# Performance work log

Measured on AMD Instinct MI355X. Metric: run time of the kernel, lower is better.

## Reference

```python
import jax, jax.numpy as jnp
import numpy as np

N_NODES = 100000
N_EDGES = 1600000
IN_F = 128
HID = 16
NEG_SLOPE = 0.2


def setup_inputs() -> dict:
    key = jax.random.key(0)
    ks = jax.random.split(key, 12)
    x = jax.random.normal(ks[0], (N_NODES, IN_F), dtype=jnp.float32)
    edge_index = jax.random.randint(ks[1], (2, N_EDGES), 0, N_NODES, dtype=jnp.int32)
    s1 = 1.0 / np.sqrt(IN_F)
    s2 = 1.0 / np.sqrt(2 * HID)
    # layer 1: heads=2, out=16, concat -> 32
    W1 = jax.random.normal(ks[2], (IN_F, 2 * HID), dtype=jnp.float32) * s1
    a_src1 = jax.random.normal(ks[3], (2, HID), dtype=jnp.float32) * s2
    a_dst1 = jax.random.normal(ks[4], (2, HID), dtype=jnp.float32) * s2
    b1 = jnp.zeros((2 * HID,), dtype=jnp.float32)
    # layer 2: heads=1, out=1
    W2 = jax.random.normal(ks[5], (2 * HID, 1), dtype=jnp.float32) * s2
    a_src2 = jax.random.normal(ks[6], (1, 1), dtype=jnp.float32)
    a_dst2 = jax.random.normal(ks[7], (1, 1), dtype=jnp.float32)
    b2 = jnp.zeros((1,), dtype=jnp.float32)
    return {"x": x, "edge_index": edge_index, "W1": W1, "a_src1": a_src1,
            "a_dst1": a_dst1, "b1": b1, "W2": W2, "a_src2": a_src2,
            "a_dst2": a_dst2, "b2": b2}


def gat_conv(x, src, dst, W, a_src, a_dst, bias, heads, out_ch, concat):
    # PyG GATConv: linear proj, per-edge leaky-relu score, segment softmax over
    # incoming edges (dst), scatter-add aggregation. Self loops already in src/dst.
    n = x.shape[0]
    h = (x @ W).reshape(n, heads, out_ch)                      # [N,H,C]
    alpha_s = (h * a_src[None]).sum(-1)                        # [N,H]
    alpha_d = (h * a_dst[None]).sum(-1)                        # [N,H]
    e = jax.nn.leaky_relu(alpha_s[src] + alpha_d[dst], NEG_SLOPE)  # [E,H]
    m = jax.lax.stop_gradient(jax.ops.segment_max(e, dst, num_segments=n))
    ex = jnp.exp(e - m[dst])
    denom = jax.ops.segment_sum(ex, dst, num_segments=n)       # [N,H]
    alpha = ex / (denom[dst] + 1e-16)                          # [E,H]
    out = jax.ops.segment_sum(alpha[..., None] * h[src], dst, num_segments=n)  # [N,H,C]
    out = out.reshape(n, heads * out_ch) if concat else out.mean(axis=1)
    return out + bias


def reference(x, edge_index, W1, a_src1, a_dst1, b1, W2, a_src2, a_dst2, b2):
    n = x.shape[0]
    loop = jnp.arange(n, dtype=edge_index.dtype)
    src = jnp.concatenate([edge_index[0], loop])
    dst = jnp.concatenate([edge_index[1], loop])
    h = jax.nn.elu(gat_conv(x, src, dst, W1, a_src1, a_dst1, b1, 2, HID, True))
    out = gat_conv(h, src, dst, W2, a_src2, a_dst2, b2, 1, 1, False)
    return out
```

## Files before the change

### kernel.cpp

```cpp
#include <hip/hip_runtime.h>
#include <math.h>

#define IN_F 128
#define C1 32
#define NEG 0.2f
#define BSZ 128
#define CAP 2560
#define EPB 2048
#define TPW 2

typedef _Float16 h16;
typedef _Float16 h16x2 __attribute__((ext_vector_type(2)));
typedef _Float16 h16x4 __attribute__((ext_vector_type(4)));
typedef _Float16 h16x8 __attribute__((ext_vector_type(8)));
typedef float f32x4 __attribute__((ext_vector_type(4)));

__device__ __forceinline__ float leaky(float x) { return x >= 0.f ? x : NEG * x; }

__global__ __launch_bounds__(256)
void k_fat(const float* __restrict__ x, const float* __restrict__ W1,
           const float* __restrict__ a_s, const float* __restrict__ a_d,
           h16* __restrict__ h1h, float* __restrict__ as1,
           float* __restrict__ ad1, int N,
           const int* __restrict__ ei, int E, int ET, int nbk,
           int* __restrict__ bcnt, int* __restrict__ ebuf, int nproj) {
    __shared__ int smem[6144];
    int t = threadIdx.x;
    if ((int)blockIdx.x < nproj) {
        int wid = t >> 6, lane = t & 63;
        int q = lane >> 4, r = lane & 15;
        h16x8 Bf[2][4];
        #pragma unroll
        for (int ct = 0; ct < 2; ++ct)
            #pragma unroll
            for (int kc = 0; kc < 4; ++kc)
                #pragma unroll
                for (int j = 0; j < 8; ++j)
                    Bf[ct][kc][j] = (h16)W1[(kc * 32 + q * 8 + j) * C1 + ct * 16 + r];
        float a_s0 = a_s[r], a_s1v = a_s[16 + r];
        float a_d0 = a_d[r], a_d1v = a_d[16 + r];
        #pragma unroll
        for (int tt = 0; tt < TPW; ++tt) {
            int tile = (blockIdx.x * 4 + wid) * TPW + tt;
            int m0 = tile << 4;
            if (m0 >= N) break;
            int row = m0 + r; if (row >= N) row = N - 1;
            const float* xr = x + (size_t)row * IN_F + q * 8;
            f32x4 acc0 = {0.f, 0.f, 0.f, 0.f};
            f32x4 acc1 = {0.f, 0.f, 0.f, 0.f};
            #pragma unroll
            for (int kc = 0; kc < 4; ++kc) {
                float4 xa = *(const float4*)(xr + kc * 32);
                float4 xb = *(const float4*)(xr + kc * 32 + 4);
                h16x8 A;
                A[0] = (h16)xa.x; A[1] = (h16)xa.y; A[2] = (h16)xa.z; A[3] = (h16)xa.w;
                A[4] = (h16)xb.x; A[5] = (h16)xb.y; A[6] = (h16)xb.z; A[7] = (h16)xb.w;
                acc0 = __builtin_amdgcn_mfma_f32_16x16x32_f16(A, Bf[0][kc], acc0, 0, 0, 0);
                acc1 = __builtin_amdgcn_mfma_f32_16x16x32_f16(A, Bf[1][kc], acc1, 0, 0, 0);
            }
            #pragma unroll
            for (int reg = 0; reg < 4; ++reg) {
                int node = m0 + q * 4 + reg;
                bool vld = node < N;
                float h0 = acc0[reg], h1 = acc1[reg];
                if (vld) {
                    h1h[(size_t)node * C1 + r]      = (h16)h0;
                    h1h[(size_t)node * C1 + 16 + r] = (h16)h1;
                }
                float s0 = h0 * a_s0, s1 = h1 * a_s1v;
                float d0 = h0 * a_d0, d1 = h1 * a_d1v;
                s0 += __shfl_xor(s0, 1); s0 += __shfl_xor(s0, 2); s0 += __shfl_xor(s0, 4); s0 += __shfl_xor(s0, 8);
                s1 += __shfl_xor(s1, 1); s1 += __shfl_xor(s1, 2); s1 += __shfl_xor(s1, 4); s1 += __shfl_xor(s1, 8);
                d0 += __shfl_xor(d0, 1); d0 += __shfl_xor(d0, 2); d0 += __shfl_xor(d0, 4); d0 += __shfl_xor(d0, 8);
                d1 += __shfl_xor(d1, 1); d1 += __shfl_xor(d1, 2); d1 += __shfl_xor(d1, 4); d1 += __shfl_xor(d1, 8);
                if (vld && r == 0) {
                    *(float2*)&as1[node * 2] = make_float2(s0, s1);
                    *(float2*)&ad1[node * 2] = make_float2(d0, d1);
                }
            }
        }
    } else {
        int* hist = smem;
        int* lcur = hist + 1024;
        int2* ecache = (int2*)(lcur + 1024);
        int bid = blockIdx.x - nproj;
        hist[t] = 0; hist[t + 256] = 0; hist[t + 512] = 0; hist[t + 768] = 0;
        __syncthreads();
        int i0 = bid * EPB, i1 = min(ET, i0 + EPB);
        for (int i = i0 + t; i < i1; i += 256) {
            int s, d;
            if (i < E) { s = ei[i]; d = ei[E + i]; } else { s = d = i - E; }
            ecache[i - i0] = make_int2(s, d);
            atomicAdd(&hist[d >> 7], 1);
        }
        __syncthreads();
        for (int b = t; b < nbk; b += 256) {
            int h = hist[b];
            int base = h ? atomicAdd(&bcnt[b], h) : 0;
            lcur[b] = b * CAP + base;
        }
        __syncthreads();
        for (int i = i0 + t; i < i1; i += 256) {
            int2 e = ecache[i - i0];
            int bkt = e.y >> 7;
            int pos = atomicAdd(&lcur[bkt], 1);
            if (pos < (bkt + 1) * CAP)
                ebuf[pos] = (e.x << 7) | (e.y & 127);
        }
    }
}

__global__ __launch_bounds__(512)
void k_bagg(const int* __restrict__ bcnt, const int* __restrict__ ebuf,
            int N, int nbk, int ET,
            const float* __restrict__ as1, const float* __restrict__ ad1,
            const float* __restrict__ b1, const float* __restrict__ W2,
            const h16* __restrict__ h1h, int* __restrict__ off,
            int* __restrict__ csr1, float* __restrict__ p2) {
    __shared__ int2 elist[CAP];
    __shared__ int deg[BSZ], sst[BSZ], cur[BSZ];
    __shared__ float adl[BSZ * 2];
    __shared__ int red[8];
    int b = blockIdx.x, t = threadIdx.x;
    int cnt = min(bcnt[b], CAP);
    int ebase = b * CAP;
    int n0 = b * BSZ;
    int part = 0;
    for (int k = t; k < b; k += 512) part += min(bcnt[k], CAP);
    part += __shfl_xor(part, 1);  part += __shfl_xor(part, 2);
    part += __shfl_xor(part, 4);  part += __shfl_xor(part, 8);
    part += __shfl_xor(part, 16); part += __shfl_xor(part, 32);
    if ((t & 63) == 0) red[t >> 6] = part;
    if (t < BSZ) {
        deg[t] = 0;
        int n = n0 + t;
        float2 v = (n < N) ? ((const float2*)ad1)[n] : make_float2(0.f, 0.f);
        adl[t * 2] = v.x; adl[t * 2 + 1] = v.y;
    }
    __syncthreads();
    int fbase = red[0] + red[1] + red[2] + red[3] + red[4] + red[5] + red[6] + red[7];
    if (b == nbk - 1 && t == 0) off[N] = ET;
    for (int i = t; i < cnt; i += 512)
        atomicAdd(&deg[ebuf[ebase + i] & 127], 1);
    __syncthreads();
    int v = (t < BSZ) ? deg[t] : 0;
    __syncthreads();
    for (int o = 1; o < BSZ; o <<= 1) {
        int xv = (t >= o && t < BSZ) ? deg[t - o] : 0;
        __syncthreads();
        if (t < BSZ) deg[t] += xv;
        __syncthreads();
    }
    if (t < BSZ) {
        int excl = deg[t] - v;
        sst[t] = excl; cur[t] = excl;
        if (n0 + t < N) off[n0 + t] = fbase + excl;
    }
    __syncthreads();
    for (int i = t; i < cnt; i += 512) {
        int e = ebuf[ebase + i];
        int dl = e & 127, s = e >> 7;
        float2 asv = ((const float2*)as1)[s];
        float w0 = __expf(leaky(asv.x + adl[dl * 2 + 0]));
        float w1 = __expf(leaky(asv.y + adl[dl * 2 + 1]));
        h16x2 wp = { (h16)w0, (h16)w1 };
        int p = atomicAdd(&cur[dl], 1);
        int2 rec; rec.x = s; rec.y = *(int*)&wp;
        elist[p] = rec;
        csr1[fbase + p] = s;
    }
    __syncthreads();
    int l = t & 7, slot = t >> 3, c0 = l * 4, head = l >> 2;
    float b1l[4] = { b1[c0], b1[c0 + 1], b1[c0 + 2], b1[c0 + 3] };
    float w2l[4] = { W2[c0], W2[c0 + 1], W2[c0 + 2], W2[c0 + 3] };
    #pragma unroll
    for (int pass = 0; pass < 2; ++pass) {
        int dl = pass * 64 + slot;
        int node = n0 + dl;
        if (node >= N) break;
        int j0 = sst[dl], j1 = deg[dl];
        float den = 0.f, a0 = 0.f, a1 = 0.f, a2 = 0.f, a3 = 0.f;
        for (int j = j0; j < j1; j += 4) {
            #pragma unroll
            for (int k = 0; k < 4; ++k) {
                int jj = j + k;
                bool valid = jj < j1;
                jj = valid ? jj : j0;
                int2 e = elist[jj];
                int s = e.x;
                h16x2 wv = *(h16x2*)&e.y;
                float w = valid ? (float)(head ? wv.y : wv.x) : 0.f;
                h16x4 hv = *(const h16x4*)(h1h + ((size_t)s << 5) + c0);
                den += w;
                a0 = fmaf(w, (float)hv.x, a0);
                a1 = fmaf(w, (float)hv.y, a1);
                a2 = fmaf(w, (float)hv.z, a2);
                a3 = fmaf(w, (float)hv.w, a3);
            }
        }
        float inv = 1.f / (den + 1e-16f);
        float o, val = 0.f;
        o = a0 * inv + b1l[0]; o = o > 0.f ? o : expm1f(o); val = fmaf(o, w2l[0], val);
        o = a1 * inv + b1l[1]; o = o > 0.f ? o : expm1f(o); val = fmaf(o, w2l[1], val);
        o = a2 * inv + b1l[2]; o = o > 0.f ? o : expm1f(o); val = fmaf(o, w2l[2], val);
        o = a3 * inv + b1l[3]; o = o > 0.f ? o : expm1f(o); val = fmaf(o, w2l[3], val);
        val += __shfl_xor(val, 1); val += __shfl_xor(val, 2); val += __shfl_xor(val, 4);
        if (l == 0) p2[node] = val;
    }
}

__global__ void k_l2(const int* __restrict__ off, const int* __restrict__ csr1,
                     const float* __restrict__ p2, const float* __restrict__ as2,
                     const float* __restrict__ ad2, const float* __restrict__ b2,
                     float* __restrict__ out, int N) {
    int i = blockIdx.x * blockDim.x + threadIdx.x;
    if (i >= N) return;
    float A = as2[0];
    float Bc = ad2[0] * p2[i];
    float den = 0.f, num = 0.f;
    int j0 = off[i], j1 = off[i + 1];
    for (int j = j0; j < j1; j += 4) {
        #pragma unroll
        for (int k = 0; k < 4; ++k) {
            int jj = j + k;
            bool valid = jj < j1;
            int s = csr1[valid ? jj : j0];
            float ps = p2[s];
            float w = valid ? __expf(leaky(fmaf(ps, A, Bc))) : 0.f;
            den += w;
            num = fmaf(w, ps, num);
        }
    }
    out[i] = num / (den + 1e-16f) + b2[0];
}

extern "C" void kernel_launch(void* const* d_in, const int* in_sizes, int n_in,
                              void* d_out, int out_size, void* d_ws, size_t ws_size,
                              hipStream_t stream) {
    const float* x    = (const float*)d_in[0];
    const int*   ei   = (const int*)d_in[1];
    const float* W1   = (const float*)d_in[2];
    const float* a_s1 = (const float*)d_in[3];
    const float* a_d1 = (const float*)d_in[4];
    const float* b1   = (const float*)d_in[5];
    const float* W2   = (const float*)d_in[6];
    const float* a_s2 = (const float*)d_in[7];
    const float* a_d2 = (const float*)d_in[8];
    const float* b2   = (const float*)d_in[9];
    float* out = (float*)d_out;

    const int N  = in_sizes[0] / IN_F;
    const int E  = in_sizes[1] / 2;
    const int ET = E + N;
    const int nbk = (N + BSZ - 1) / BSZ;

    float* w   = (float*)d_ws;
    float* as1 = w; w += (size_t)2 * N;
    float* ad1 = w; w += (size_t)2 * N;
    float* p2  = w; w += (size_t)N;
    h16* h1h   = (h16*)w;
    w += (size_t)16 * N;
    int* iw     = (int*)w;
    int* bcnt   = iw; iw += 1024;
    int* off    = iw; iw += (N + 1);
    int* csr1   = iw; iw += ET;
    int* ebuf   = iw; iw += (size_t)nbk * CAP;

    const int B = 256;
    const int ntile = (N + 15) / 16;
    const int nproj = (ntile + 4 * TPW - 1) / (4 * TPW);
    const int nblkA = (ET + EPB - 1) / EPB;

    hipMemsetAsync(bcnt, 0, 1024 * sizeof(int), stream);
    k_fat <<<nproj + nblkA, B, 0, stream>>>(x, W1, a_s1, a_d1, h1h, as1, ad1, N,
                                            ei, E, ET, nbk, bcnt, ebuf, nproj);
    k_bagg<<<nbk, 512, 0, stream>>>(bcnt, ebuf, N, nbk, ET, as1, ad1, b1, W2,
                                    h1h, off, csr1, p2);
    k_l2  <<<(N + B - 1) / B, B, 0, stream>>>(off, csr1, p2, a_s2, a_d2, b2, out, N);
}
```

Before: 181.9 us.

## Partition bucket counters eight ways, drop edge LDS cache, use 8 lanes per node in layer 2

The edge binning now spreads each destination bucket across 8 sub-partitions, each with its own global counter and region, so fewer blocks contend on the same atomic counter. The shared-memory edge cache is removed and edges are re-read from global memory instead, which cuts LDS use and may raise occupancy. The layer-1 aggregation loop is unrolled by 8, and layer 2 assigns 8 lanes per node with a shuffle reduction instead of one thread per node. In exchange, the edge indices are read twice, the bucket buffer is larger and sparser, and each partition now caps at 512 edges per bucket, so edges beyond that are silently dropped.

```diff
diff --git a/kernel.cpp b/kernel.cpp
--- a/kernel.cpp
+++ b/kernel.cpp
@@ -5,7 +5,10 @@
 #define C1 32
 #define NEG 0.2f
 #define BSZ 128
-#define CAP 2560
+#define P 8
+#define CAPP 512
+#define CAPT 4096
+#define ECAP 4096
 #define EPB 2048
 #define TPW 2
 
@@ -24,7 +27,7 @@
            float* __restrict__ ad1, int N,
            const int* __restrict__ ei, int E, int ET, int nbk,
            int* __restrict__ bcnt, int* __restrict__ ebuf, int nproj) {
-    __shared__ int smem[6144];
+    __shared__ int smem[2048];
     int t = threadIdx.x;
     if ((int)blockIdx.x < nproj) {
         int wid = t >> 6, lane = t & 63;
@@ -81,31 +84,30 @@
         }
     } else {
         int* hist = smem;
-        int* lcur = hist + 1024;
-        int2* ecache = (int2*)(lcur + 1024);
+        int* lcur = smem + 1024;
         int bid = blockIdx.x - nproj;
+        int part = bid & (P - 1);
         hist[t] = 0; hist[t + 256] = 0; hist[t + 512] = 0; hist[t + 768] = 0;
         __syncthreads();
         int i0 = bid * EPB, i1 = min(ET, i0 + EPB);
+        for (int i = i0 + t; i < i1; i += 256) {
+            int d = (i < E) ? ei[E + i] : (i - E);
+            atomicAdd(&hist[d >> 7], 1);
+        }
+        __syncthreads();
+        for (int b = t; b < nbk; b += 256) {
+            int h = hist[b];
+            int base = h ? atomicAdd(&bcnt[(b << 3) | part], h) : 0;
+            lcur[b] = (b << 12) + (part << 9) + base;
+        }
+        __syncthreads();
         for (int i = i0 + t; i < i1; i += 256) {
             int s, d;
             if (i < E) { s = ei[i]; d = ei[E + i]; } else { s = d = i - E; }
-            ecache[i - i0] = make_int2(s, d);
-            atomicAdd(&hist[d >> 7], 1);
-        }
-        __syncthreads();
-        for (int b = t; b < nbk; b += 256) {
-            int h = hist[b];
-            int base = h ? atomicAdd(&bcnt[b], h) : 0;
-            lcur[b] = b * CAP + base;
-        }
-        __syncthreads();
-        for (int i = i0 + t; i < i1; i += 256) {
-            int2 e = ecache[i - i0];
-            int bkt = e.y >> 7;
+            int bkt = d >> 7;
             int pos = atomicAdd(&lcur[bkt], 1);
-            if (pos < (bkt + 1) * CAP)
-                ebuf[pos] = (e.x << 7) | (e.y & 127);
+            if (pos - ((bkt << 12) + (part << 9)) < CAPP)
+                ebuf[pos] = (s << 7) | (d & 127);
         }
     }
 }
@@ -117,16 +119,19 @@
             const float* __restrict__ b1, const float* __restrict__ W2,
             const h16* __restrict__ h1h, int* __restrict__ off,
             int* __restrict__ csr1, float* __restrict__ p2) {
-    __shared__ int2 elist[CAP];
+    __shared__ int2 elist[ECAP];
     __shared__ int deg[BSZ], sst[BSZ], cur[BSZ];
     __shared__ float adl[BSZ * 2];
     __shared__ int red[8];
     int b = blockIdx.x, t = threadIdx.x;
-    int cnt = min(bcnt[b], CAP);
-    int ebase = b * CAP;
     int n0 = b * BSZ;
     int part = 0;
-    for (int k = t; k < b; k += 512) part += min(bcnt[k], CAP);
+    for (int k = t; k < b; k += 512) {
+        const int4* q = (const int4*)(bcnt + (k << 3));
+        int4 c0 = q[0], c1 = q[1];
+        part += min(c0.x, CAPP) + min(c0.y, CAPP) + min(c0.z, CAPP) + min(c0.w, CAPP)
+              + min(c1.x, CAPP) + min(c1.y, CAPP) + min(c1.z, CAPP) + min(c1.w, CAPP);
+    }
     part += __shfl_xor(part, 1);  part += __shfl_xor(part, 2);
     part += __shfl_xor(part, 4);  part += __shfl_xor(part, 8);
     part += __shfl_xor(part, 16); part += __shfl_xor(part, 32);
@@ -140,8 +145,16 @@
     __syncthreads();
     int fbase = red[0] + red[1] + red[2] + red[3] + red[4] + red[5] + red[6] + red[7];
     if (b == nbk - 1 && t == 0) off[N] = ET;
-    for (int i = t; i < cnt; i += 512)
-        atomicAdd(&deg[ebuf[ebase + i] & 127], 1);
+    const int4* qb = (const int4*)(bcnt + (b << 3));
+    int4 cb0 = qb[0], cb1 = qb[1];
+    int cnt_p[8] = { min(cb0.x, CAPP), min(cb0.y, CAPP), min(cb0.z, CAPP), min(cb0.w, CAPP),
+                     min(cb1.x, CAPP), min(cb1.y, CAPP), min(cb1.z, CAPP), min(cb1.w, CAPP) };
+    #pragma unroll
+    for (int p = 0; p < 8; ++p) {
+        int eb = (b << 12) + (p << 9);
+        for (int i = t; i < cnt_p[p]; i += 512)
+            atomicAdd(&deg[ebuf[eb + i] & 127], 1);
+    }
     __syncthreads();
     int v = (t < BSZ) ? deg[t] : 0;
     __syncthreads();
@@ -157,17 +170,21 @@
         if (n0 + t < N) off[n0 + t] = fbase + excl;
     }
     __syncthreads();
-    for (int i = t; i < cnt; i += 512) {
-        int e = ebuf[ebase + i];
-        int dl = e & 127, s = e >> 7;
-        float2 asv = ((const float2*)as1)[s];
-        float w0 = __expf(leaky(asv.x + adl[dl * 2 + 0]));
-        float w1 = __expf(leaky(asv.y + adl[dl * 2 + 1]));
-        h16x2 wp = { (h16)w0, (h16)w1 };
-        int p = atomicAdd(&cur[dl], 1);
-        int2 rec; rec.x = s; rec.y = *(int*)&wp;
-        elist[p] = rec;
-        csr1[fbase + p] = s;
+    #pragma unroll
+    for (int p = 0; p < 8; ++p) {
+        int eb = (b << 12) + (p << 9);
+        for (int i = t; i < cnt_p[p]; i += 512) {
+            int e = ebuf[eb + i];
+            int dl = e & 127, s = e >> 7;
+            float2 asv = ((const float2*)as1)[s];
+            float w0 = __expf(leaky(asv.x + adl[dl * 2 + 0]));
+            float w1 = __expf(leaky(asv.y + adl[dl * 2 + 1]));
+            h16x2 wp = { (h16)w0, (h16)w1 };
+            int pos = atomicAdd(&cur[dl], 1);
+            int2 rec; rec.x = s; rec.y = *(int*)&wp;
+            elist[pos] = rec;
+            csr1[fbase + pos] = s;
+        }
     }
     __syncthreads();
     int l = t & 7, slot = t >> 3, c0 = l * 4, head = l >> 2;
@@ -180,9 +197,9 @@
         if (node >= N) break;
         int j0 = sst[dl], j1 = deg[dl];
         float den = 0.f, a0 = 0.f, a1 = 0.f, a2 = 0.f, a3 = 0.f;
-        for (int j = j0; j < j1; j += 4) {
-            #pragma unroll
-            for (int k = 0; k < 4; ++k) {
+        for (int j = j0; j < j1; j += 8) {
+            #pragma unroll
+            for (int k = 0; k < 8; ++k) {
                 int jj = j + k;
                 bool valid = jj < j1;
                 jj = valid ? jj : j0;
@@ -209,29 +226,27 @@
     }
 }
 
-__global__ void k_l2(const int* __restrict__ off, const int* __restrict__ csr1,
-                     const float* __restrict__ p2, const float* __restrict__ as2,
-                     const float* __restrict__ ad2, const float* __restrict__ b2,
-                     float* __restrict__ out, int N) {
-    int i = blockIdx.x * blockDim.x + threadIdx.x;
-    if (i >= N) return;
+__global__ __launch_bounds__(256)
+void k_l2(const int* __restrict__ off, const int* __restrict__ csr1,
+          const float* __restrict__ p2, const float* __restrict__ as2,
+          const float* __restrict__ ad2, const float* __restrict__ b2,
+          float* __restrict__ out, int N) {
+    int tid = blockIdx.x * 256 + threadIdx.x;
+    int g = tid >> 3, l = tid & 7;
+    if (g >= N) return;
     float A = as2[0];
-    float Bc = ad2[0] * p2[i];
+    float Bc = ad2[0] * p2[g];
     float den = 0.f, num = 0.f;
-    int j0 = off[i], j1 = off[i + 1];
-    for (int j = j0; j < j1; j += 4) {
-        #pragma unroll
-        for (int k = 0; k < 4; ++k) {
-            int jj = j + k;
-            bool valid = jj < j1;
-            int s = csr1[valid ? jj : j0];
-            float ps = p2[s];
-            float w = valid ? __expf(leaky(fmaf(ps, A, Bc))) : 0.f;
-            den += w;
-            num = fmaf(w, ps, num);
-        }
-    }
-    out[i] = num / (den + 1e-16f) + b2[0];
+    int j0 = off[g], j1 = off[g + 1];
+    for (int j = j0 + l; j < j1; j += 8) {
+        float ps = p2[csr1[j]];
+        float w = __expf(leaky(fmaf(ps, A, Bc)));
+        den += w;
+        num = fmaf(w, ps, num);
+    }
+    den += __shfl_xor(den, 1); den += __shfl_xor(den, 2); den += __shfl_xor(den, 4);
+    num += __shfl_xor(num, 1); num += __shfl_xor(num, 2); num += __shfl_xor(num, 4);
+    if (l == 0) out[g] = num / (den + 1e-16f) + b2[0];
 }
 
 extern "C" void kernel_launch(void* const* d_in, const int* in_sizes, int n_in,
@@ -261,20 +276,20 @@
     h16* h1h   = (h16*)w;
     w += (size_t)16 * N;
     int* iw     = (int*)w;
-    int* bcnt   = iw; iw += 1024;
+    int* bcnt   = iw; iw += 8192;
     int* off    = iw; iw += (N + 1);
     int* csr1   = iw; iw += ET;
-    int* ebuf   = iw; iw += (size_t)nbk * CAP;
+    int* ebuf   = iw; iw += (size_t)nbk * CAPT;
 
     const int B = 256;
     const int ntile = (N + 15) / 16;
     const int nproj = (ntile + 4 * TPW - 1) / (4 * TPW);
     const int nblkA = (ET + EPB - 1) / EPB;
 
-    hipMemsetAsync(bcnt, 0, 1024 * sizeof(int), stream);
+    hipMemsetAsync(bcnt, 0, 8192 * sizeof(int), stream);
     k_fat <<<nproj + nblkA, B, 0, stream>>>(x, W1, a_s1, a_d1, h1h, as1, ad1, N,
                                             ei, E, ET, nbk, bcnt, ebuf, nproj);
     k_bagg<<<nbk, 512, 0, stream>>>(bcnt, ebuf, N, nbk, ET, as1, ad1, b1, W2,
                                     h1h, off, csr1, p2);
-    k_l2  <<<(N + B - 1) / B, B, 0, stream>>>(off, csr1, p2, a_s2, a_d2, b2, out, N);
-}
+    k_l2  <<<(N * 8 + B - 1) / B, B, 0, stream>>>(off, csr1, p2, a_s2, a_d2, b2, out, N);
+}
```

New measurement: 189.6 us. 4.2% more time.
